# Performance work log

Measured on AMD Instinct MI355X. Metric: run time of the kernel, lower is better.

## Reference

```python
import jax, jax.numpy as jnp
import numpy as np

N_NODES = 50000
HIDDEN = 128
N_EDGES = 1_600_000


def gcn_conv(x, W, b, src, dst, n_nodes):
    """PyG GCNConv: linear, add self-loops, symmetric deg^-1/2 normalization, scatter-sum."""
    h = x @ W  # [N, D]
    # degree with self-loops: 1 + in-degree from edges (edge weight 1)
    deg = jnp.ones((n_nodes,), h.dtype).at[dst].add(1.0)
    dinv = jax.lax.rsqrt(deg)  # deg^{-1/2}, deg >= 1 so no inf
    # neighbor messages: norm_e = dinv[src] * dinv[dst]
    msgs = h[src] * (dinv[src] * dinv[dst])[:, None]  # [E, D]
    agg = jnp.zeros_like(h).at[dst].add(msgs)
    # self-loop contribution: norm = dinv[i]*dinv[i]
    agg = agg + h * (dinv * dinv)[:, None]
    return agg + b


def setup_inputs() -> dict:
    key = jax.random.key(0)
    ks = jax.random.split(key, 7)
    x = jax.random.normal(ks[0], (N_NODES, HIDDEN), dtype=jnp.float32)
    edge_index = jax.random.randint(ks[1], (2, N_EDGES), 0, N_NODES, dtype=jnp.int64)
    s = 1.0 / np.sqrt(HIDDEN)
    W1 = jax.random.uniform(ks[2], (HIDDEN, HIDDEN), jnp.float32, -s, s)
    b1 = jax.random.uniform(ks[3], (HIDDEN,), jnp.float32, -s, s)
    W2 = jax.random.uniform(ks[4], (HIDDEN, HIDDEN), jnp.float32, -s, s)
    b2 = jax.random.uniform(ks[5], (HIDDEN,), jnp.float32, -s, s)
    return {"x": x, "edge_index": edge_index, "W1": W1, "b1": b1, "W2": W2, "b2": b2}


def reference(x, edge_index, W1, b1, W2, b2):
    src, dst = edge_index[0], edge_index[1]
    h = jax.nn.relu(gcn_conv(x, W1, b1, src, dst, N_NODES))
    z = gcn_conv(h, W2, b2, src, dst, N_NODES)
    return z
```

## Files before the change

kernel.cpp:

```cpp
#include <hip/hip_runtime.h>
#include <hip/hip_fp16.h>
#include <type_traits>

#define D 128


__global__ __launch_bounds__(256) void deg_kernel(const int* __restrict__ dst,
                                                  int* __restrict__ deg,
                                                  int* __restrict__ rank, int E) {
  int t = blockIdx.x * 256 + threadIdx.x;
  int e0 = t * 8;
  if (e0 + 8 <= E) {
    int4 a = *reinterpret_cast<const int4*>(dst + e0);
    int4 b = *reinterpret_cast<const int4*>(dst + e0 + 4);
    int4 ra, rb;
    ra.x = atomicAdd(&deg[a.x], 1);
    ra.y = atomicAdd(&deg[a.y], 1);
    ra.z = atomicAdd(&deg[a.z], 1);
    ra.w = atomicAdd(&deg[a.w], 1);
    rb.x = atomicAdd(&deg[b.x], 1);
    rb.y = atomicAdd(&deg[b.y], 1);
    rb.z = atomicAdd(&deg[b.z], 1);
    rb.w = atomicAdd(&deg[b.w], 1);
    *reinterpret_cast<int4*>(rank + e0) = ra;
    *reinterpret_cast<int4*>(rank + e0 + 4) = rb;
  } else {
    for (int e = e0; e < E; ++e) rank[e] = atomicAdd(&deg[dst[e]], 1);
  }
}


__global__ __launch_bounds__(256) void bsum_kernel(const int* __restrict__ deg,
                                                   int* __restrict__ bsum) {
  __shared__ int ws[4];
  int i0 = blockIdx.x * 1024 + threadIdx.x * 4;
  int4 v = *reinterpret_cast<const int4*>(deg + i0);
  int s = v.x + v.y + v.z + v.w;
  #pragma unroll
  for (int off = 32; off; off >>= 1) s += __shfl_down(s, off);
  if ((threadIdx.x & 63) == 0) ws[threadIdx.x >> 6] = s;
  __syncthreads();
  if (threadIdx.x == 0) bsum[blockIdx.x] = ws[0] + ws[1] + ws[2] + ws[3];
}


__global__ __launch_bounds__(256) void scan_kernel(const int* __restrict__ deg,
                                                   const int* __restrict__ bsum,
                                                   int* __restrict__ offsets,
                                                   float* __restrict__ dinv,
                                                   int N, int E) {
  __shared__ int ts[256];
  int b = blockIdx.x;
  int base = 0;
  for (int t = 0; t < b; ++t) base += bsum[t];

  int i0 = b * 1024 + threadIdx.x * 4;
  int4 v = *reinterpret_cast<const int4*>(deg + i0);
  int t4 = v.x + v.y + v.z + v.w;
  ts[threadIdx.x] = t4;
  __syncthreads();
  #pragma unroll
  for (int off = 1; off < 256; off <<= 1) {
    int u = (threadIdx.x >= off) ? ts[threadIdx.x - off] : 0;
    __syncthreads();
    ts[threadIdx.x] += u;
    __syncthreads();
  }
  int run = base + ts[threadIdx.x] - t4;

  int dd[4] = {v.x, v.y, v.z, v.w};
  #pragma unroll
  for (int k = 0; k < 4; ++k) {
    int i = i0 + k;
    if (i < N) {
      offsets[i] = run;
      dinv[i] = rsqrtf(1.0f + (float)dd[k]);
    }
    run += dd[k];
  }
  if (b == 0 && threadIdx.x == 0) offsets[N] = E;
}


__global__ __launch_bounds__(256) void place_kernel(const int* __restrict__ src,
                                                    const int* __restrict__ dst,
                                                    const int* __restrict__ rank,
                                                    const int* __restrict__ offsets,
                                                    const float* __restrict__ dinv,
                                                    unsigned int* __restrict__ csr, int E) {
  int t = blockIdx.x * 256 + threadIdx.x;
  int e0 = t * 4;
  if (e0 + 4 <= E) {
    int4 s4 = *reinterpret_cast<const int4*>(src + e0);
    int4 d4 = *reinterpret_cast<const int4*>(dst + e0);
    int4 r4 = *reinterpret_cast<const int4*>(rank + e0);
    int ss[4] = {s4.x, s4.y, s4.z, s4.w};
    int dd[4] = {d4.x, d4.y, d4.z, d4.w};
    int rr[4] = {r4.x, r4.y, r4.z, r4.w};
    int pos[4];
    float nm[4];
    #pragma unroll
    for (int k = 0; k < 4; ++k) pos[k] = offsets[dd[k]] + rr[k];
    #pragma unroll
    for (int k = 0; k < 4; ++k) nm[k] = dinv[ss[k]] * dinv[dd[k]];
    #pragma unroll
    for (int k = 0; k < 4; ++k) {
      unsigned int q = (unsigned int)__float2int_rn(nm[k] * 32767.0f);
      csr[pos[k]] = ((unsigned int)ss[k] << 15) | q;
    }
  } else {
    for (int e = e0; e < E; ++e) {
      int s = src[e];
      int d = dst[e];
      int pos = offsets[d] + rank[e];
      float nm = dinv[s] * dinv[d];
      unsigned int q = (unsigned int)__float2int_rn(nm * 32767.0f);
      csr[pos] = ((unsigned int)s << 15) | q;
    }
  }
}


template <typename TI>
__global__ __launch_bounds__(256) void gemm_kernel(const TI* __restrict__ X,
                                                   const float* __restrict__ W,
                                                   __half* __restrict__ H, int N) {
  __shared__ float xs[32 * D];
  int row0 = blockIdx.x * 32;
  if constexpr (std::is_same<TI, float>::value) {
    #pragma unroll
    for (int jj = 0; jj < 4; ++jj) {
      int f4 = threadIdx.x + jj * 256;
      int r = f4 >> 5;
      float4 v = make_float4(0.f, 0.f, 0.f, 0.f);
      if (row0 + r < N) v = *reinterpret_cast<const float4*>(X + (size_t)row0 * D + (size_t)f4 * 4);
      *reinterpret_cast<float4*>(xs + f4 * 4) = v;
    }
  } else {
    #pragma unroll
    for (int jj = 0; jj < 2; ++jj) {
      int g8 = threadIdx.x + jj * 256;
      int r = g8 >> 4;
      uint4 raw = make_uint4(0u, 0u, 0u, 0u);
      if (row0 + r < N)
        raw = *reinterpret_cast<const uint4*>((const __half*)X + (size_t)row0 * D + (size_t)g8 * 8);
      const __half2* hp = reinterpret_cast<const __half2*>(&raw);
      float* dst8 = xs + (size_t)g8 * 8;
      #pragma unroll
      for (int k = 0; k < 4; ++k) {
        float2 f = __half22float2(hp[k]);
        dst8[k * 2] = f.x;
        dst8[k * 2 + 1] = f.y;
      }
    }
  }
  __syncthreads();

  int tx = threadIdx.x & 63;
  int ty = threadIdx.x >> 6;
  int c0 = tx * 2;
  float2 acc[8];
  #pragma unroll
  for (int r = 0; r < 8; ++r) acc[r] = make_float2(0.f, 0.f);
  const float* xbase = xs + ty * 8 * D;

  for (int k = 0; k < D; k += 4) {
    float2 w0 = *reinterpret_cast<const float2*>(W + (size_t)(k + 0) * D + c0);
    float2 w1 = *reinterpret_cast<const float2*>(W + (size_t)(k + 1) * D + c0);
    float2 w2 = *reinterpret_cast<const float2*>(W + (size_t)(k + 2) * D + c0);
    float2 w3 = *reinterpret_cast<const float2*>(W + (size_t)(k + 3) * D + c0);
    #pragma unroll
    for (int r = 0; r < 8; ++r) {
      float4 xv = *reinterpret_cast<const float4*>(xbase + r * D + k);
      acc[r].x = fmaf(xv.x, w0.x, acc[r].x); acc[r].y = fmaf(xv.x, w0.y, acc[r].y);
      acc[r].x = fmaf(xv.y, w1.x, acc[r].x); acc[r].y = fmaf(xv.y, w1.y, acc[r].y);
      acc[r].x = fmaf(xv.z, w2.x, acc[r].x); acc[r].y = fmaf(xv.z, w2.y, acc[r].y);
      acc[r].x = fmaf(xv.w, w3.x, acc[r].x); acc[r].y = fmaf(xv.w, w3.y, acc[r].y);
    }
  }

  #pragma unroll
  for (int r = 0; r < 8; ++r) {
    int row = row0 + ty * 8 + r;
    if (row < N)
      *reinterpret_cast<__half2*>(H + (size_t)row * D + c0) = __floats2half2_rn(acc[r].x, acc[r].y);
  }
}


template <int DO_RELU, typename TO>
__global__ __launch_bounds__(256) void agg_kernel(const __half* __restrict__ H,
                                                  const int* __restrict__ offsets,
                                                  const unsigned int* __restrict__ csr,
                                                  const float* __restrict__ dinv,
                                                  const float* __restrict__ bias,
                                                  TO* __restrict__ out, int N) {
  int n = blockIdx.x * 4 + (threadIdx.x >> 6);
  if (n >= N) return;
  int lane = threadIdx.x & 63;
  int g = lane >> 4;
  int l = lane & 15;

  int beg = offsets[n];
  int end = offsets[n + 1];

  float acc[8];
  #pragma unroll
  for (int k = 0; k < 8; ++k) acc[k] = 0.f;

  const __half* Hl = H + l * 8;

  int j = beg + g;
  for (; j + 4 < end; j += 8) {
    unsigned int p0 = csr[j];
    unsigned int p1 = csr[j + 4];
    float m0 = (float)(p0 & 0x7fffu) * (1.0f / 32767.0f);
    float m1 = (float)(p1 & 0x7fffu) * (1.0f / 32767.0f);
    uint4 r0 = *reinterpret_cast<const uint4*>(Hl + (size_t)(p0 >> 15) * D);
    uint4 r1 = *reinterpret_cast<const uint4*>(Hl + (size_t)(p1 >> 15) * D);
    const __half2* h0 = reinterpret_cast<const __half2*>(&r0);
    const __half2* h1 = reinterpret_cast<const __half2*>(&r1);
    #pragma unroll
    for (int k = 0; k < 4; ++k) {
      float2 f0 = __half22float2(h0[k]);
      float2 f1 = __half22float2(h1[k]);
      acc[2 * k]     = fmaf(f0.x, m0, acc[2 * k]);
      acc[2 * k + 1] = fmaf(f0.y, m0, acc[2 * k + 1]);
      acc[2 * k]     = fmaf(f1.x, m1, acc[2 * k]);
      acc[2 * k + 1] = fmaf(f1.y, m1, acc[2 * k + 1]);
    }
  }
  if (j < end) {
    unsigned int p0 = csr[j];
    float m0 = (float)(p0 & 0x7fffu) * (1.0f / 32767.0f);
    uint4 r0 = *reinterpret_cast<const uint4*>(Hl + (size_t)(p0 >> 15) * D);
    const __half2* h0 = reinterpret_cast<const __half2*>(&r0);
    #pragma unroll
    for (int k = 0; k < 4; ++k) {
      float2 f0 = __half22float2(h0[k]);
      acc[2 * k]     = fmaf(f0.x, m0, acc[2 * k]);
      acc[2 * k + 1] = fmaf(f0.y, m0, acc[2 * k + 1]);
    }
  }

  #pragma unroll
  for (int k = 0; k < 8; ++k) {
    acc[k] += __shfl_xor(acc[k], 16);
    acc[k] += __shfl_xor(acc[k], 32);
  }

  if (g == 0) {
    float di = dinv[n];
    float dii = di * di;
    uint4 rs = *reinterpret_cast<const uint4*>(Hl + (size_t)n * D);
    const __half2* hs = reinterpret_cast<const __half2*>(&rs);
    float4 bv0 = *reinterpret_cast<const float4*>(bias + l * 8);
    float4 bv1 = *reinterpret_cast<const float4*>(bias + l * 8 + 4);
    float v[8];
    #pragma unroll
    for (int k = 0; k < 4; ++k) {
      float2 f = __half22float2(hs[k]);
      v[2 * k]     = fmaf(f.x, dii, acc[2 * k]);
      v[2 * k + 1] = fmaf(f.y, dii, acc[2 * k + 1]);
    }
    v[0] += bv0.x; v[1] += bv0.y; v[2] += bv0.z; v[3] += bv0.w;
    v[4] += bv1.x; v[5] += bv1.y; v[6] += bv1.z; v[7] += bv1.w;
    if (DO_RELU) {
      #pragma unroll
      for (int k = 0; k < 8; ++k) v[k] = fmaxf(v[k], 0.f);
    }
    if constexpr (std::is_same<TO, float>::value) {
      float4 o0 = make_float4(v[0], v[1], v[2], v[3]);
      float4 o1 = make_float4(v[4], v[5], v[6], v[7]);
      *reinterpret_cast<float4*>(out + (size_t)n * D + l * 8) = o0;
      *reinterpret_cast<float4*>(out + (size_t)n * D + l * 8 + 4) = o1;
    } else {
      uint4 pk;
      __half2 q0 = __floats2half2_rn(v[0], v[1]);
      __half2 q1 = __floats2half2_rn(v[2], v[3]);
      __half2 q2 = __floats2half2_rn(v[4], v[5]);
      __half2 q3 = __floats2half2_rn(v[6], v[7]);
      pk.x = *reinterpret_cast<unsigned int*>(&q0);
      pk.y = *reinterpret_cast<unsigned int*>(&q1);
      pk.z = *reinterpret_cast<unsigned int*>(&q2);
      pk.w = *reinterpret_cast<unsigned int*>(&q3);
      *reinterpret_cast<uint4*>((__half*)out + (size_t)n * D + l * 8) = pk;
    }
  }
}


extern "C" void kernel_launch(void* const* d_in, const int* in_sizes, int n_in,
                              void* d_out, int out_size, void* d_ws, size_t ws_size,
                              hipStream_t stream) {
  const float* x  = (const float*)d_in[0];
  const int* edge = (const int*)d_in[1];
  const float* W1 = (const float*)d_in[2];
  const float* b1 = (const float*)d_in[3];
  const float* W2 = (const float*)d_in[4];
  const float* b2 = (const float*)d_in[5];
  const int N = in_sizes[0] / D;
  const int E = in_sizes[1] / 2;
  const int* srcp = edge;
  const int* dstp = edge + E;
  float* out = (float*)d_out;

  const int NP = (N + 1023) & ~1023;
  const int SB = NP / 1024;

  auto align = [](size_t v) { return (v + 255) & ~(size_t)255; };
  char* ws = (char*)d_ws;
  size_t o = 0;
  int*   deg     = (int*)(ws + o);             o += align((size_t)NP * 4);
  int*   bsum    = (int*)(ws + o);             o += align((size_t)SB * 4);
  int*   offsets = (int*)(ws + o);             o += align((size_t)(N + 1) * 4);
  int*   rank    = (int*)(ws + o);             o += align((size_t)((E + 7) & ~7) * 4);
  float* dinv    = (float*)(ws + o);           o += align((size_t)N * 4);
  unsigned int* csr = (unsigned int*)(ws + o); o += align((size_t)E * 4);
  __half* Hh     = (__half*)(ws + o);          o += align((size_t)N * D * 2);
  __half* h1h    = (__half*)(ws + o);          o += align((size_t)N * D * 2);

  hipMemsetAsync(deg, 0, (size_t)NP * 4, stream);
  int deg_threads = (E + 7) / 8;
  deg_kernel<<<(deg_threads + 255) / 256, 256, 0, stream>>>(dstp, deg, rank, E);
  bsum_kernel<<<SB, 256, 0, stream>>>(deg, bsum);
  scan_kernel<<<SB, 256, 0, stream>>>(deg, bsum, offsets, dinv, N, E);
  int pl_threads = (E + 3) / 4;
  place_kernel<<<(pl_threads + 255) / 256, 256, 0, stream>>>(srcp, dstp, rank, offsets, dinv, csr, E);

  int gemm_blocks = (N + 31) / 32;
  int agg_blocks = (N + 3) / 4;

  gemm_kernel<float><<<gemm_blocks, 256, 0, stream>>>(x, W1, Hh, N);
  agg_kernel<1, __half><<<agg_blocks, 256, 0, stream>>>(Hh, offsets, csr, dinv, b1, h1h, N);

  gemm_kernel<__half><<<gemm_blocks, 256, 0, stream>>>(h1h, W2, Hh, N);
  agg_kernel<0, float><<<agg_blocks, 256, 0, stream>>>(Hh, offsets, csr, dinv, b2, out, N);
}
```

Baseline: 286.6 us.

## Fuse first GEMM with degree counting and unroll aggregation gather to four edges

Merges the degree/rank atomic kernel into the first GEMM launch as extra blocks, so the independent GEMM and the degree counting share one grid and can overlap. The degree part now handles one edge per thread instead of eight vectorized edges. The aggregation loop is also unrolled to issue four neighbor row gathers per iteration, with a loop for the remainder, to raise memory-level parallelism. The costs are higher register use in the aggregation kernel and GEMM blocks that use shared memory sitting in the same grid as the lightweight atomic blocks.

```diff
diff --git a/kernel.cpp b/kernel.cpp
--- a/kernel.cpp
+++ b/kernel.cpp
@@ -3,31 +3,6 @@
 #include <type_traits>
 
 #define D 128
-
-
-__global__ __launch_bounds__(256) void deg_kernel(const int* __restrict__ dst,
-                                                  int* __restrict__ deg,
-                                                  int* __restrict__ rank, int E) {
-  int t = blockIdx.x * 256 + threadIdx.x;
-  int e0 = t * 8;
-  if (e0 + 8 <= E) {
-    int4 a = *reinterpret_cast<const int4*>(dst + e0);
-    int4 b = *reinterpret_cast<const int4*>(dst + e0 + 4);
-    int4 ra, rb;
-    ra.x = atomicAdd(&deg[a.x], 1);
-    ra.y = atomicAdd(&deg[a.y], 1);
-    ra.z = atomicAdd(&deg[a.z], 1);
-    ra.w = atomicAdd(&deg[a.w], 1);
-    rb.x = atomicAdd(&deg[b.x], 1);
-    rb.y = atomicAdd(&deg[b.y], 1);
-    rb.z = atomicAdd(&deg[b.z], 1);
-    rb.w = atomicAdd(&deg[b.w], 1);
-    *reinterpret_cast<int4*>(rank + e0) = ra;
-    *reinterpret_cast<int4*>(rank + e0 + 4) = rb;
-  } else {
-    for (int e = e0; e < E; ++e) rank[e] = atomicAdd(&deg[dst[e]], 1);
-  }
-}
 
 
 __global__ __launch_bounds__(256) void bsum_kernel(const int* __restrict__ deg,
@@ -122,11 +97,11 @@
 
 
 template <typename TI>
-__global__ __launch_bounds__(256) void gemm_kernel(const TI* __restrict__ X,
-                                                   const float* __restrict__ W,
-                                                   __half* __restrict__ H, int N) {
+__device__ __forceinline__ void gemm_body(const TI* __restrict__ X,
+                                          const float* __restrict__ W,
+                                          __half* __restrict__ H, int N, int bid) {
   __shared__ float xs[32 * D];
-  int row0 = blockIdx.x * 32;
+  int row0 = bid * 32;
   if constexpr (std::is_same<TI, float>::value) {
     #pragma unroll
     for (int jj = 0; jj < 4; ++jj) {
@@ -188,6 +163,27 @@
 }
 
 
+__global__ __launch_bounds__(256) void fused_gemm_deg_kernel(
+    const float* __restrict__ X, const float* __restrict__ W,
+    __half* __restrict__ H, int N, int GB,
+    const int* __restrict__ dst, int* __restrict__ deg,
+    int* __restrict__ rank, int E) {
+  if ((int)blockIdx.x < GB) {
+    gemm_body<float>(X, W, H, N, blockIdx.x);
+  } else {
+    int e = (blockIdx.x - GB) * 256 + threadIdx.x;
+    if (e < E) rank[e] = atomicAdd(&deg[dst[e]], 1);
+  }
+}
+
+
+__global__ __launch_bounds__(256) void gemm_h_kernel(const __half* __restrict__ X,
+                                                     const float* __restrict__ W,
+                                                     __half* __restrict__ H, int N) {
+  gemm_body<__half>(X, W, H, N, blockIdx.x);
+}
+
+
 template <int DO_RELU, typename TO>
 __global__ __launch_bounds__(256) void agg_kernel(const __half* __restrict__ H,
                                                   const int* __restrict__ offsets,
@@ -211,26 +207,40 @@
   const __half* Hl = H + l * 8;
 
   int j = beg + g;
-  for (; j + 4 < end; j += 8) {
+  for (; j + 12 < end; j += 16) {
     unsigned int p0 = csr[j];
     unsigned int p1 = csr[j + 4];
+    unsigned int p2 = csr[j + 8];
+    unsigned int p3 = csr[j + 12];
     float m0 = (float)(p0 & 0x7fffu) * (1.0f / 32767.0f);
     float m1 = (float)(p1 & 0x7fffu) * (1.0f / 32767.0f);
+    float m2 = (float)(p2 & 0x7fffu) * (1.0f / 32767.0f);
+    float m3 = (float)(p3 & 0x7fffu) * (1.0f / 32767.0f);
     uint4 r0 = *reinterpret_cast<const uint4*>(Hl + (size_t)(p0 >> 15) * D);
     uint4 r1 = *reinterpret_cast<const uint4*>(Hl + (size_t)(p1 >> 15) * D);
+    uint4 r2 = *reinterpret_cast<const uint4*>(Hl + (size_t)(p2 >> 15) * D);
+    uint4 r3 = *reinterpret_cast<const uint4*>(Hl + (size_t)(p3 >> 15) * D);
     const __half2* h0 = reinterpret_cast<const __half2*>(&r0);
     const __half2* h1 = reinterpret_cast<const __half2*>(&r1);
+    const __half2* h2 = reinterpret_cast<const __half2*>(&r2);
+    const __half2* h3 = reinterpret_cast<const __half2*>(&r3);
     #pragma unroll
     for (int k = 0; k < 4; ++k) {
       float2 f0 = __half22float2(h0[k]);
       float2 f1 = __half22float2(h1[k]);
+      float2 f2 = __half22float2(h2[k]);
+      float2 f3 = __half22float2(h3[k]);
       acc[2 * k]     = fmaf(f0.x, m0, acc[2 * k]);
       acc[2 * k + 1] = fmaf(f0.y, m0, acc[2 * k + 1]);
       acc[2 * k]     = fmaf(f1.x, m1, acc[2 * k]);
       acc[2 * k + 1] = fmaf(f1.y, m1, acc[2 * k + 1]);
-    }
-  }
-  if (j < end) {
+      acc[2 * k]     = fmaf(f2.x, m2, acc[2 * k]);
+      acc[2 * k + 1] = fmaf(f2.y, m2, acc[2 * k + 1]);
+      acc[2 * k]     = fmaf(f3.x, m3, acc[2 * k]);
+      acc[2 * k + 1] = fmaf(f3.y, m3, acc[2 * k + 1]);
+    }
+  }
+  for (; j < end; j += 4) {
     unsigned int p0 = csr[j];
     float m0 = (float)(p0 & 0x7fffu) * (1.0f / 32767.0f);
     uint4 r0 = *reinterpret_cast<const uint4*>(Hl + (size_t)(p0 >> 15) * D);
@@ -314,26 +324,27 @@
   int*   deg     = (int*)(ws + o);             o += align((size_t)NP * 4);
   int*   bsum    = (int*)(ws + o);             o += align((size_t)SB * 4);
   int*   offsets = (int*)(ws + o);             o += align((size_t)(N + 1) * 4);
-  int*   rank    = (int*)(ws + o);             o += align((size_t)((E + 7) & ~7) * 4);
+  int*   rank    = (int*)(ws + o);             o += align((size_t)E * 4);
   float* dinv    = (float*)(ws + o);           o += align((size_t)N * 4);
   unsigned int* csr = (unsigned int*)(ws + o); o += align((size_t)E * 4);
   __half* Hh     = (__half*)(ws + o);          o += align((size_t)N * D * 2);
   __half* h1h    = (__half*)(ws + o);          o += align((size_t)N * D * 2);
 
+  int gemm_blocks = (N + 31) / 32;
+  int deg_blocks  = (E + 255) / 256;
+  int agg_blocks  = (N + 3) / 4;
+
   hipMemsetAsync(deg, 0, (size_t)NP * 4, stream);
-  int deg_threads = (E + 7) / 8;
-  deg_kernel<<<(deg_threads + 255) / 256, 256, 0, stream>>>(dstp, deg, rank, E);
+  fused_gemm_deg_kernel<<<gemm_blocks + deg_blocks, 256, 0, stream>>>(
+      x, W1, Hh, N, gemm_blocks, dstp, deg, rank, E);
+
   bsum_kernel<<<SB, 256, 0, stream>>>(deg, bsum);
   scan_kernel<<<SB, 256, 0, stream>>>(deg, bsum, offsets, dinv, N, E);
   int pl_threads = (E + 3) / 4;
   place_kernel<<<(pl_threads + 255) / 256, 256, 0, stream>>>(srcp, dstp, rank, offsets, dinv, csr, E);
 
-  int gemm_blocks = (N + 31) / 32;
-  int agg_blocks = (N + 3) / 4;
-
-  gemm_kernel<float><<<gemm_blocks, 256, 0, stream>>>(x, W1, Hh, N);
   agg_kernel<1, __half><<<agg_blocks, 256, 0, stream>>>(Hh, offsets, csr, dinv, b1, h1h, N);
 
-  gemm_kernel<__half><<<gemm_blocks, 256, 0, stream>>>(h1h, W2, Hh, N);
+  gemm_h_kernel<<<gemm_blocks, 256, 0, stream>>>(h1h, W2, Hh, N);
   agg_kernel<0, float><<<agg_blocks, 256, 0, stream>>>(Hh, offsets, csr, dinv, b2, out, N);
 }
```

After: 288.6 us. No clear change (+0.7%).
